# Kernel tuning notes

Measured on AMD Instinct MI355X. Metric: run time of the kernel, lower is better.

The kernel has to match this reference:

```python
import jax, jax.numpy as jnp
import numpy as np

B, P, E, D, A, M, V, T = 64, 196, 2048, 512, 512, 512, 10000, 31


def setup_inputs() -> dict:
    key = jax.random.key(0)
    ks = jax.random.split(key, 20)
    s = 0.02
    inp = {
        "encoder_out": jax.random.normal(ks[0], (B, P, E), jnp.float32),
        "captions": jax.random.randint(ks[1], (B, T), 0, V),
        "caption_lengths": jax.random.randint(ks[2], (B,), 2, T + 1).at[0].set(T),
        # parameters
        "W_emb": jax.random.normal(ks[3], (V, M), jnp.float32) * s,
        "We": jax.random.normal(ks[4], (A, E), jnp.float32) * s,
        "be": jnp.zeros((A,), jnp.float32),
        "Wd": jax.random.normal(ks[5], (A, D), jnp.float32) * s,
        "bd": jnp.zeros((A,), jnp.float32),
        "wf": jax.random.normal(ks[6], (1, A), jnp.float32) * s,
        "bf": jnp.zeros((1,), jnp.float32),
        "Wih": jax.random.normal(ks[7], (4 * D, M + E), jnp.float32) * s,
        "bih": jnp.zeros((4 * D,), jnp.float32),
        "Whh": jax.random.normal(ks[8], (4 * D, D), jnp.float32) * s,
        "bhh": jnp.zeros((4 * D,), jnp.float32),
        "Wfc": jax.random.normal(ks[9], (V, D), jnp.float32) * s,
        "bfc": jnp.zeros((V,), jnp.float32),
        "Wh0": jax.random.normal(ks[10], (D, E), jnp.float32) * s,
        "bh0": jnp.zeros((D,), jnp.float32),
        "Wc0": jax.random.normal(ks[11], (D, E), jnp.float32) * s,
        "bc0": jnp.zeros((D,), jnp.float32),
    }
    return inp


def _decode(encoder_out, W_emb, We, be, Wd, bd, wf, bf, Wih, bih, Whh, bhh,
            Wfc, bfc, Wh0, bh0, Wc0, bc0, captions, caption_lengths):
    # sort by length descending (matches torch .sort(descending=True))
    idx = jnp.argsort(-caption_lengths)
    lens = caption_lengths[idx]
    enc = encoder_out[idx]              # [B,P,E]
    caps = captions[idx]                # [B,T]
    emb = W_emb[caps]                   # [B,T,M]
    mean_enc = enc.mean(axis=1)         # [B,E]
    h0 = mean_enc @ Wh0.T + bh0         # [B,D]
    c0 = mean_enc @ Wc0.T + bc0
    dec_len = lens - 1                  # [B]
    att1 = enc @ We.T + be              # [B,P,A] precomputed encoder projection
    Tmax = caps.shape[1] - 1

    def step(carry, xs):
        h, c = carry
        e_t, t = xs                     # e_t: [B,M]
        active = (t < dec_len)          # [B]
        att2 = h @ Wd.T + bd            # [B,A]
        scores = jnp.tanh(att1 + att2[:, None, :]) @ wf[0] + bf[0]  # [B,P]
        alpha = jax.nn.softmax(scores, axis=-1)                      # [B,P]
        ctx = jnp.einsum('bp,bpe->be', alpha, enc)                   # [B,E]
        x = jnp.concatenate([e_t, ctx], axis=-1)                     # [B,M+E]
        gates = x @ Wih.T + bih + h @ Whh.T + bhh                    # [B,4D]
        i_g, f_g, g_g, o_g = jnp.split(gates, 4, axis=-1)
        c_t = jax.nn.sigmoid(f_g) * c + jax.nn.sigmoid(i_g) * jnp.tanh(g_g)
        h_t = jax.nn.sigmoid(o_g) * jnp.tanh(c_t)
        pred = h_t @ Wfc.T + bfc        # dropout in eval mode = identity
        m = active[:, None]
        h_new = jnp.where(m, h_t, h)
        c_new = jnp.where(m, c_t, c)
        pred = jnp.where(m, pred, 0.0)
        alpha = jnp.where(m, alpha, 0.0)
        return (h_new, c_new), (pred, alpha)

    emb_ts = jnp.swapaxes(emb[:, :Tmax, :], 0, 1)  # [Tmax,B,M]
    ts = jnp.arange(Tmax)
    _, (preds, alphas) = jax.lax.scan(step, (h0, c0), (emb_ts, ts))
    predictions = jnp.swapaxes(preds, 0, 1)   # [B,Tmax,V]
    alphas = jnp.swapaxes(alphas, 0, 1)       # [B,Tmax,P]
    return predictions, alphas


def reference(encoder_out, captions, caption_lengths, W_emb, We, be, Wd, bd,
              wf, bf, Wih, bih, Whh, bhh, Wfc, bfc, Wh0, bh0, Wc0, bc0):
    return _decode(encoder_out, W_emb, We, be, Wd, bd, wf, bf, Wih, bih,
                   Whh, bhh, Wfc, bfc, Wh0, bh0, Wc0, bc0,
                   captions, caption_lengths)
```

## Files before the change

### kernel.cpp

```cpp
#include <hip/hip_runtime.h>
#include <cstdint>
#include <cstddef>

typedef __attribute__((ext_vector_type(8))) short short8;
typedef __attribute__((ext_vector_type(4))) float f32x4;

#define DEV static __device__ __forceinline__

#define PRED_ELEMS 19200000ULL

#define OFF_ENC   0ULL
#define OFF_ATT1  51380224ULL
#define OFF_B1    64225280ULL
#define OFF_WFC   69468160ULL
#define OFF_WEB   79724544ULL
#define OFF_B0    81821696ULL
#define OFF_HH    81821696ULL
#define OFF_B2    86016000ULL
#define OFF_HX    94404608ULL
#define OFF_C     94535680ULL
#define OFF_ATT2  94666752ULL
#define OFF_GEH   94797824ULL
#define OFF_SC    95322112ULL
#define OFF_CTX   95372288ULL
#define OFF_META  95634432ULL
#define OFF_ENCW  96000000ULL
#define ENCW_BYTES 51380224ULL

DEV float b2f(unsigned short u){ unsigned v = ((unsigned)u) << 16; float f; __builtin_memcpy(&f, &v, 4); return f; }
DEV unsigned short f2b(float x){ unsigned v; __builtin_memcpy(&v, &x, 4); unsigned r = v + 0x7fffu + ((v >> 16) & 1u); return (unsigned short)(r >> 16); }
DEV float sigm(float x){ return 1.0f / (1.0f + __expf(-x)); }
DEV float tanhf_fast(float x){ float e = __expf(2.0f * x); return 1.0f - 2.0f / (e + 1.0f); }

DEV void gload16(const void* g, void* l){
  __builtin_amdgcn_global_load_lds((const __attribute__((address_space(1))) unsigned int*)g,
                                   (__attribute__((address_space(3))) unsigned int*)l, 16, 0, 0);
}

DEV void mm_core(const unsigned short* A, int ldA, int m0,
                 const unsigned short* Bm, int ldB, int n0,
                 int kIters, unsigned short* As, unsigned short* Bs, f32x4 acc[4])
{
  const int tid = threadIdx.x;
  const int lane = tid & 63, w = tid >> 6;
  const unsigned short* ga = A + (size_t)(m0 + lane) * ldA + w * 8;
  const unsigned short* gb = Bm + (size_t)(n0 + lane) * ldB + w * 8;
  unsigned short* la = As + w * 512;
  unsigned short* lb = Bs + w * 512;
  const int kb = lane >> 4, rr = lane & 15;
  for (int kk = 0; kk < kIters; ++kk) {
    gload16(ga, la); gload16(gb, lb);
    ga += 32; gb += 32;
    asm volatile("s_waitcnt vmcnt(0)" ::: "memory");
    __syncthreads();
    short8 bfr = *(const short8*)(Bs + (size_t)(kb * 64 + w * 16 + rr) * 8);
#pragma unroll
    for (int f = 0; f < 4; ++f) {
      short8 afr = *(const short8*)(As + (size_t)(kb * 64 + f * 16 + rr) * 8);
      acc[f] = __builtin_amdgcn_mfma_f32_16x16x32_bf16(afr, bfr, acc[f], 0, 0, 0);
    }
    __syncthreads();
  }
}

__global__ void k_meta(const int* __restrict__ caps, const int* __restrict__ lens, int* __restrict__ meta){
  int j = threadIdx.x;
  int lj = lens[j];
  int rank = 0;
  for (int k = 0; k < 64; ++k) { int lk = lens[k]; rank += (lk > lj) || (lk == lj && k < j); }
  meta[rank] = j; meta[64 + rank] = lj - 1;
  for (int t = 0; t < 31; ++t) meta[160 + rank * 31 + t] = caps[j * 31 + t];
  __syncthreads();
  if (j < 30) { int c = 0; for (int b = 0; b < 64; ++b) c += (meta[64 + b] > j); meta[128 + j] = c; }
}

__global__ __launch_bounds__(256) void k_encg(const float* __restrict__ enc, const int* __restrict__ meta, unsigned short* __restrict__ encb){
  int row = blockIdx.x; int b = row / 196, p = row % 196;
  const float* src = enc + ((size_t)meta[b] * 196 + p) * 2048;
  unsigned short* dst = encb + (size_t)row * 2048;
  int e0 = threadIdx.x * 8;
  short8 o;
#pragma unroll
  for (int j = 0; j < 8; ++j) o[j] = (short)f2b(src[e0 + j]);
  *(short8*)(dst + e0) = o;
}

__global__ __launch_bounds__(256) void k_wconv(const float* We, const float* Wh0, const float* Wc0,
                        const float* Wd, const float* Whh, const float* Wih, const float* Wfc,
                        unsigned short* Web, unsigned short* B0, unsigned short* B1,
                        unsigned short* Wfcb, unsigned short* B2){
  int bid = blockIdx.x, tid = threadIdx.x;
  if (bid < 512) {
    const float* s = We + (size_t)bid * 2048; unsigned short* d = Web + (size_t)bid * 2048;
    int e0 = tid * 8; short8 o;
#pragma unroll
    for (int j = 0; j < 8; ++j) o[j] = (short)f2b(s[e0 + j]);
    *(short8*)(d + e0) = o;
  } else if (bid < 1536) {
    int r = bid - 512;
    const float* s = (r < 512) ? (Wh0 + (size_t)r * 2048) : (Wc0 + (size_t)(r - 512) * 2048);
    unsigned short* d = B0 + (size_t)r * 2048;
    int e0 = tid * 8; short8 o;
#pragma unroll
    for (int j = 0; j < 8; ++j) o[j] = (short)f2b(s[e0 + j]);
    *(short8*)(d + e0) = o;
  } else if (bid < 3584) {
    int jr = bid - 1536; int g = (jr & 3) * 512 + (jr >> 2);
    const float* s = Wih + (size_t)g * 2560 + 512;
    unsigned short* d = B2 + (size_t)jr * 2048;
    int e0 = tid * 8; short8 o;
#pragma unroll
    for (int j = 0; j < 8; ++j) o[j] = (short)f2b(s[e0 + j]);
    *(short8*)(d + e0) = o;
  } else if (bid < 6144) {
    int n = bid - 3584; unsigned short* d = B1 + (size_t)n * 1024;
    int k0 = tid * 4;
    if (n < 512) {
#pragma unroll
      for (int j = 0; j < 4; ++j) { int k = k0 + j; d[k] = (k < 512) ? f2b(Wd[(size_t)n * 512 + k]) : (unsigned short)0; }
    } else {
      int j2 = n - 512; int g = (j2 & 3) * 512 + (j2 >> 2);
#pragma unroll
      for (int j = 0; j < 4; ++j) { int k = k0 + j;
        d[k] = (k < 512) ? f2b(Whh[(size_t)g * 512 + k]) : f2b(Wih[(size_t)g * 2560 + (k - 512)]); }
    }
  } else {
    int v = bid - 6144; unsigned short* d = Wfcb + (size_t)v * 512;
    int k0 = tid * 2;
#pragma unroll
    for (int j = 0; j < 2; ++j) d[k0 + j] = (v < 10000) ? f2b(Wfc[(size_t)v * 512 + k0 + j]) : (unsigned short)0;
  }
}

__global__ __launch_bounds__(256) void k_mean(const unsigned short* __restrict__ encb, unsigned short* __restrict__ meanb){
  int b = blockIdx.y, ch = blockIdx.x;
  int e = ch * 512 + threadIdx.x * 2;
  const unsigned short* ep = encb + (size_t)b * 196 * 2048 + e;
  float s0 = 0.f, s1 = 0.f;
  for (int p = 0; p < 196; ++p) {
    unsigned u = *(const unsigned*)(ep + (size_t)p * 2048);
    s0 += b2f((unsigned short)(u & 0xffff));
    s1 += b2f((unsigned short)(u >> 16));
  }
  const float inv = 1.0f / 196.0f;
  unsigned o = ((unsigned)f2b(s1 * inv) << 16) | f2b(s0 * inv);
  *(unsigned*)(meanb + (size_t)b * 2048 + e) = o;
}

__global__ __launch_bounds__(256) void k_h0c0(const unsigned short* meanb, const unsigned short* B0,
                      const float* bh0, const float* bc0, unsigned short* hx, float* cbuf){
  __shared__ __align__(16) unsigned short As[2048], Bs[2048];
  f32x4 acc[4];
#pragma unroll
  for (int f = 0; f < 4; ++f) acc[f] = (f32x4){0.f,0.f,0.f,0.f};
  int nt = blockIdx.x;
  mm_core(meanb, 2048, 0, B0, 2048, nt * 64, 64, As, Bs, acc);
  int lane = threadIdx.x & 63, w = threadIdx.x >> 6;
  int col = lane & 15, rhi = lane >> 4;
  int n = nt * 64 + w * 16 + col;
#pragma unroll
  for (int f = 0; f < 4; ++f)
#pragma unroll
    for (int r = 0; r < 4; ++r) {
      int b = f * 16 + rhi * 4 + r; float v = acc[f][r];
      if (n < 512) hx[(size_t)b * 1024 + n] = f2b(v + bh0[n]);
      else cbuf[(size_t)b * 512 + (n - 512)] = v + bc0[n - 512];
    }
}

__global__ void k_emb0(const float* __restrict__ Wemb, const int* __restrict__ meta, unsigned short* __restrict__ hx){
  int b = blockIdx.x;
  int cap = meta[160 + b * 31];
  for (int j = threadIdx.x; j < 512; j += 256)
    hx[(size_t)b * 1024 + 512 + j] = f2b(Wemb[(size_t)cap * 512 + j]);
}

__global__ __launch_bounds__(256) void k_att1(const unsigned short* __restrict__ encb,
                      const unsigned short* __restrict__ Web,
                      const float* __restrict__ be, unsigned short* __restrict__ att1b){
  __shared__ __align__(16) unsigned short As[2][4096], Bs[2][4096];
  int tid = threadIdx.x, lane = tid & 63, w = tid >> 6;
  int bid = blockIdx.x, mt, nt;
  if (bid < 384) { mt = (bid >> 5) * 8 + (bid & 7); nt = (bid >> 3) & 3; }
  else           { mt = 96 + ((bid - 384) >> 2);    nt = (bid - 384) & 3; }
  int wr = (w >> 1) * 64, wc = (w & 1) * 64;
  int rr = lane & 15, kb = lane >> 4;
  f32x4 acc[4][4];
#pragma unroll
  for (int f = 0; f < 4; ++f)
#pragma unroll
    for (int q = 0; q < 4; ++q) acc[f][q] = (f32x4){0.f,0.f,0.f,0.f};

  const unsigned short* gA = encb + (size_t)mt * 128 * 2048;
  const unsigned short* gB = Web + (size_t)nt * 128 * 2048;
  int L0 = tid, L1 = tid + 256;
  size_t s0 = (size_t)(L0 & 127) * 2048 + ((L0 >> 7) << 3);
  size_t s1 = (size_t)(L1 & 127) * 2048 + ((L1 >> 7) << 3);
  int d0 = (w * 64) * 8, d1 = (w * 64 + 256) * 8;

#define STAGE_A1(kk, bf) do { \
    gload16(gA + s0 + (size_t)(kk) * 32, &As[bf][d0]); \
    gload16(gB + s0 + (size_t)(kk) * 32, &Bs[bf][d0]); \
    gload16(gA + s1 + (size_t)(kk) * 32, &As[bf][d1]); \
    gload16(gB + s1 + (size_t)(kk) * 32, &Bs[bf][d1]); \
  } while (0)

  STAGE_A1(0, 0);
  __syncthreads();
  for (int kk = 0; kk < 64; ++kk) {
    int cur = kk & 1;
    if (kk < 63) STAGE_A1(kk + 1, cur ^ 1);
    short8 af[4], bq[4];
#pragma unroll
    for (int f = 0; f < 4; ++f)
      af[f] = *(const short8*)&As[cur][((kb << 7) + wr + f * 16 + rr) * 8];
#pragma unroll
    for (int q = 0; q < 4; ++q)
      bq[q] = *(const short8*)&Bs[cur][((kb << 7) + wc + q * 16 + rr) * 8];
#pragma unroll
    for (int f = 0; f < 4; ++f)
#pragma unroll
      for (int q = 0; q < 4; ++q)
        acc[f][q] = __builtin_amdgcn_mfma_f32_16x16x32_bf16(af[f], bq[q], acc[f][q], 0, 0, 0);
    __syncthreads();
  }
#undef STAGE_A1
  int col = lane & 15, rhi = lane >> 4;
#pragma unroll
  for (int q = 0; q < 4; ++q) {
    int n = nt * 128 + wc + q * 16 + col;
    float bev = be[n];
#pragma unroll
    for (int f = 0; f < 4; ++f)
#pragma unroll
      for (int r = 0; r < 4; ++r) {
        int m = mt * 128 + wr + f * 16 + rhi * 4 + r;
        att1b[(size_t)m * 512 + n] = f2b(acc[f][q][r] + bev);
      }
  }
}

__global__ __launch_bounds__(256) void k_encw(const unsigned short* __restrict__ encb,
                      const unsigned short* __restrict__ B2, unsigned short* __restrict__ encW){
  __shared__ __align__(16) unsigned short As[2][4096], Bs[2][4096];
  int tid = threadIdx.x, lane = tid & 63, w = tid >> 6;
  int mt = blockIdx.x >> 4, nt = blockIdx.x & 15;
  int wr = (w >> 1) * 64, wc = (w & 1) * 64;
  int rr = lane & 15, kb = lane >> 4;
  f32x4 acc[4][4];
#pragma unroll
  for (int f = 0; f < 4; ++f)
#pragma unroll
    for (int q = 0; q < 4; ++q) acc[f][q] = (f32x4){0.f,0.f,0.f,0.f};

  const unsigned short* gA = encb + (size_t)mt * 128 * 2048;
  const unsigned short* gB = B2 + (size_t)nt * 128 * 2048;
  int L0 = tid, L1 = tid + 256;
  size_t s0 = (size_t)(L0 & 127) * 2048 + ((L0 >> 7) << 3);
  size_t s1 = (size_t)(L1 & 127) * 2048 + ((L1 >> 7) << 3);
  int d0 = (w * 64) * 8, d1 = (w * 64 + 256) * 8;

#define STAGE_W(kk, bf) do { \
    gload16(gA + s0 + (size_t)(kk) * 32, &As[bf][d0]); \
    gload16(gB + s0 + (size_t)(kk) * 32, &Bs[bf][d0]); \
    gload16(gA + s1 + (size_t)(kk) * 32, &As[bf][d1]); \
    gload16(gB + s1 + (size_t)(kk) * 32, &Bs[bf][d1]); \
  } while (0)

  STAGE_W(0, 0);
  __syncthreads();
  for (int kk = 0; kk < 64; ++kk) {
    int cur = kk & 1;
    if (kk < 63) STAGE_W(kk + 1, cur ^ 1);
    short8 af[4], bq[4];
#pragma unroll
    for (int f = 0; f < 4; ++f)
      af[f] = *(const short8*)&As[cur][((kb << 7) + wr + f * 16 + rr) * 8];
#pragma unroll
    for (int q = 0; q < 4; ++q)
      bq[q] = *(const short8*)&Bs[cur][((kb << 7) + wc + q * 16 + rr) * 8];
#pragma unroll
    for (int f = 0; f < 4; ++f)
#pragma unroll
      for (int q = 0; q < 4; ++q)
        acc[f][q] = __builtin_amdgcn_mfma_f32_16x16x32_bf16(af[f], bq[q], acc[f][q], 0, 0, 0);
    __syncthreads();
  }
#undef STAGE_W
  int col = lane & 15, rhi = lane >> 4;
#pragma unroll
  for (int q = 0; q < 4; ++q) {
    int n = nt * 128 + wc + q * 16 + col;
#pragma unroll
    for (int f = 0; f < 4; ++f)
#pragma unroll
      for (int r = 0; r < 4; ++r) {
        int m = mt * 128 + wr + f * 16 + rhi * 4 + r;
        encW[(size_t)m * 2048 + n] = f2b(acc[f][q][r]);
      }
  }
}

__global__ __launch_bounds__(256) void k_step1lite(const unsigned short* __restrict__ hx,
                       const unsigned short* __restrict__ B1,
                       const float* __restrict__ bd, const float* __restrict__ bih, const float* __restrict__ bhh,
                       float* __restrict__ att2f, float* __restrict__ geh){
  int w = threadIdx.x >> 6, lane = threadIdx.x & 63;
  int omega = blockIdx.x * 4 + w;
  int rr = lane & 15, kb8 = (lane >> 4) * 8;
  const unsigned short* pb; int kIt;
  if (omega < 32) { pb = B1 + (size_t)(omega * 16 + rr) * 1024 + kb8; kIt = 16; }
  else            { pb = B1 + (size_t)(512 + (omega - 32) * 16 + rr) * 1024 + kb8; kIt = 32; }
  const unsigned short* pa0 = hx + (size_t)rr * 1024 + kb8;
  f32x4 acc[4];
#pragma unroll
  for (int f = 0; f < 4; ++f) acc[f] = (f32x4){0.f,0.f,0.f,0.f};
#pragma unroll 4
  for (int kk = 0; kk < kIt; ++kk) {
    short8 bfr = *(const short8*)(pb + kk * 32);
#pragma unroll
    for (int f = 0; f < 4; ++f) {
      short8 afr = *(const short8*)(pa0 + (size_t)f * 16384 + kk * 32);
      acc[f] = __builtin_amdgcn_mfma_f32_16x16x32_bf16(afr, bfr, acc[f], 0, 0, 0);
    }
  }
  int col = lane & 15, rhi = lane >> 4;
  if (omega < 32) {
    int n = omega * 16 + col; float bv = bd[n];
#pragma unroll
    for (int f = 0; f < 4; ++f)
#pragma unroll
      for (int r = 0; r < 4; ++r) { int b = f * 16 + rhi * 4 + r; att2f[(size_t)b * 512 + n] = acc[f][r] + bv; }
  } else {
    int j = (omega - 32) * 16 + col; int g = (j & 3) * 512 + (j >> 2);
    float bv = bih[g] + bhh[g];
#pragma unroll
    for (int f = 0; f < 4; ++f)
#pragma unroll
      for (int r = 0; r < 4; ++r) { int b = f * 16 + rhi * 4 + r; geh[(size_t)b * 2048 + j] = acc[f][r] + bv; }
  }
}

__global__ __launch_bounds__(256) void k_scores(int t, const unsigned short* __restrict__ att1b, const float* __restrict__ att2f,
                        const float* __restrict__ wf, const float* __restrict__ bfp,
                        const int* __restrict__ meta, float* __restrict__ sc){
  int b = blockIdx.y, pc = blockIdx.x;
  if (b >= meta[128 + t]) return;
  int tid = threadIdx.x, lane = tid & 63, w = tid >> 6;
  float wfr[8], a2[8];
#pragma unroll
  for (int j = 0; j < 8; ++j) { wfr[j] = wf[lane * 8 + j]; a2[j] = att2f[(size_t)b * 512 + lane * 8 + j]; }
  float bf0 = bfp[0];
  for (int pi = w; pi < 49; pi += 4) {
    int p = pc * 49 + pi;
    short8 av = *(const short8*)(att1b + ((size_t)(b * 196 + p)) * 512 + lane * 8);
    float s = 0.f;
#pragma unroll
    for (int j = 0; j < 8; ++j) s += tanhf_fast(b2f((unsigned short)av[j]) + a2[j]) * wfr[j];
#pragma unroll
    for (int off = 32; off; off >>= 1) s += __shfl_xor(s, off);
    if (lane == 0) sc[(size_t)b * 196 + p] = s + bf0;
  }
}

__global__ __launch_bounds__(256) void k_gc(int t, const float* __restrict__ sc,
                      const unsigned short* __restrict__ encW, const float* __restrict__ geh,
                      const float* __restrict__ Wemb, const int* __restrict__ meta,
                      float* __restrict__ out, float* __restrict__ cbuf,
                      unsigned short* __restrict__ hx, unsigned short* __restrict__ hh){
  int b = blockIdx.y, ch = blockIdx.x;
  int tid = threadIdx.x, lane = tid & 63, w = tid >> 6;
  int na = meta[128 + t];
  __shared__ float sal[200];
  __shared__ float red[256];
  __shared__ float part[4][512];
  __shared__ float gt[512];

  if (b < na) {
    float v = (tid < 196) ? sc[(size_t)b * 196 + tid] : -3.0e38f;
    red[tid] = v; __syncthreads();
    for (int s = 128; s; s >>= 1) { if (tid < s) red[tid] = fmaxf(red[tid], red[tid + s]); __syncthreads(); }
    float mx = red[0]; __syncthreads();
    float ex = (tid < 196) ? __expf(v - mx) : 0.f;
    red[tid] = ex; __syncthreads();
    for (int s = 128; s; s >>= 1) { if (tid < s) red[tid] += red[tid + s]; __syncthreads(); }
    float inv = 1.0f / red[0];
    __syncthreads();
    if (tid < 196) {
      float al = ex * inv;
      sal[tid] = al;
      if (ch == 0) out[PRED_ELEMS + ((size_t)b * 30 + t) * 196 + tid] = al;
    }
    __syncthreads();

    const unsigned short* ep = encW + ((size_t)b * 196) * 2048 + ch * 512 + lane * 8;
    float s8[8];
#pragma unroll
    for (int j = 0; j < 8; ++j) s8[j] = 0.f;
#pragma unroll 7
    for (int i = 0; i < 49; ++i) {
      int p = w + i * 4;
      short8 vv = *(const short8*)(ep + (size_t)p * 2048);
      float a = sal[p];
#pragma unroll
      for (int j = 0; j < 8; ++j) s8[j] += a * b2f((unsigned short)vv[j]);
    }
#pragma unroll
    for (int j = 0; j < 8; ++j) part[w][lane * 8 + j] = s8[j];
    __syncthreads();
    int j0 = tid * 2;
    gt[j0]     = part[0][j0] + part[1][j0] + part[2][j0] + part[3][j0]
               + geh[(size_t)b * 2048 + ch * 512 + j0];
    gt[j0 + 1] = part[0][j0 + 1] + part[1][j0 + 1] + part[2][j0 + 1] + part[3][j0 + 1]
               + geh[(size_t)b * 2048 + ch * 512 + j0 + 1];
    __syncthreads();

    if (tid < 128) {
      int d = ch * 128 + tid;
      float ig = gt[tid * 4 + 0];
      float fg = gt[tid * 4 + 1];
      float gg = gt[tid * 4 + 2];
      float og = gt[tid * 4 + 3];
      float c0 = cbuf[(size_t)b * 512 + d];
      float ct = sigm(fg) * c0 + sigm(ig) * tanhf_fast(gg);
      float ht = sigm(og) * tanhf_fast(ct);
      cbuf[(size_t)b * 512 + d] = ct;
      unsigned short hb = f2b(ht);
      hx[(size_t)b * 1024 + d] = hb;
      hh[((size_t)t * 64 + b) * 512 + d] = hb;
      int cap = meta[160 + b * 31 + t + 1];
      hx[(size_t)b * 1024 + 512 + d] = f2b(Wemb[(size_t)cap * 512 + d]);
    }
  } else {
    if (tid < 128) {
      int d = ch * 128 + tid;
      unsigned short hold = hx[(size_t)b * 1024 + d];
      hh[((size_t)t * 64 + b) * 512 + d] = hold;
      int cap = meta[160 + b * 31 + t + 1];
      hx[(size_t)b * 1024 + 512 + d] = f2b(Wemb[(size_t)cap * 512 + d]);
    }
  }
}

__global__ __launch_bounds__(256) void k_ctx(int t, const float* __restrict__ sc, const unsigned short* __restrict__ encb,
                     const int* __restrict__ meta, float* __restrict__ out, unsigned short* __restrict__ ctxb){
  int b = blockIdx.y, ch = blockIdx.x;
  if (b >= meta[128 + t]) return;
  int tid = threadIdx.x;
  __shared__ float red[256];
  __shared__ float sal[200];
  __shared__ float part[4][512];
  float v = (tid < 196) ? sc[(size_t)b * 196 + tid] : -3.0e38f;
  red[tid] = v; __syncthreads();
  for (int s = 128; s; s >>= 1) { if (tid < s) red[tid] = fmaxf(red[tid], red[tid + s]); __syncthreads(); }
  float mx = red[0]; __syncthreads();
  float ex = (tid < 196) ? __expf(v - mx) : 0.f;
  red[tid] = ex; __syncthreads();
  for (int s = 128; s; s >>= 1) { if (tid < s) red[tid] += red[tid + s]; __syncthreads(); }
  float inv = 1.0f / red[0];
  if (tid < 196) {
    float al = ex * inv;
    sal[tid] = al;
    if (ch == 0) out[PRED_ELEMS + ((size_t)b * 30 + t) * 196 + tid] = al;
  }
  __syncthreads();
  int w = tid >> 6, lane = tid & 63;
  const unsigned short* ep = encb + (size_t)b * 196 * 2048 + ch * 512 + lane * 8;
  float s8[8];
#pragma unroll
  for (int j = 0; j < 8; ++j) s8[j] = 0.f;
#pragma unroll 7
  for (int i = 0; i < 49; ++i) {
    int p = w + i * 4;
    short8 vv = *(const short8*)(ep + (size_t)p * 2048);
    float a = sal[p];
#pragma unroll
    for (int j = 0; j < 8; ++j) s8[j] += a * b2f((unsigned short)vv[j]);
  }
#pragma unroll
  for (int j = 0; j < 8; ++j) part[w][lane * 8 + j] = s8[j];
  __syncthreads();
  float r0 = part[0][tid * 2] + part[1][tid * 2] + part[2][tid * 2] + part[3][tid * 2];
  float r1 = part[0][tid * 2 + 1] + part[1][tid * 2 + 1] + part[2][tid * 2 + 1] + part[3][tid * 2 + 1];
  unsigned o = ((unsigned)f2b(r1) << 16) | f2b(r0);
  *(unsigned*)(ctxb + (size_t)b * 2048 + ch * 512 + tid * 2) = o;
}

__global__ __launch_bounds__(256) void k_step2(int t, const unsigned short* __restrict__ ctxb,
                       const unsigned short* __restrict__ B2, const float* __restrict__ geh,
                       const float* __restrict__ Wemb, const int* __restrict__ meta,
                       float* __restrict__ cbuf, unsigned short* __restrict__ hx,
                       unsigned short* __restrict__ hh){
  __shared__ float red[4][64][17];
  int w = threadIdx.x >> 6, lane = threadIdx.x & 63;
  int n0 = blockIdx.x * 16;
  int rr = lane & 15, kb8 = (lane >> 4) * 8;
  const unsigned short* pb = B2 + (size_t)(n0 + rr) * 2048 + w * 512 + kb8;
  const unsigned short* pa = ctxb + (size_t)rr * 2048 + w * 512 + kb8;
  f32x4 acc[4];
#pragma unroll
  for (int f = 0; f < 4; ++f) acc[f] = (f32x4){0.f,0.f,0.f,0.f};
#pragma unroll 4
  for (int kk = 0; kk < 16; ++kk) {
    short8 bfr = *(const short8*)(pb + kk * 32);
#pragma unroll
    for (int f = 0; f < 4; ++f) {
      short8 afr = *(const short8*)(pa + (size_t)f * 32768 + kk * 32);
      acc[f] = __builtin_amdgcn_mfma_f32_16x16x32_bf16(afr, bfr, acc[f], 0, 0, 0);
    }
  }
  int col = lane & 15, rhi = lane >> 4;
#pragma unroll
  for (int f = 0; f < 4; ++f)
#pragma unroll
    for (int r = 0; r < 4; ++r) red[w][f * 16 + rhi * 4 + r][col] = acc[f][r];
  __syncthreads();
  int b = threadIdx.x >> 2, dl = threadIdx.x & 3;
  int d = blockIdx.x * 4 + dl;
  float g4[4];
#pragma unroll
  for (int q = 0; q < 4; ++q) {
    int nl = dl * 4 + q;
    g4[q] = red[0][b][nl] + red[1][b][nl] + red[2][b][nl] + red[3][b][nl]
          + geh[(size_t)b * 2048 + n0 + nl];
  }
  float c0 = cbuf[(size_t)b * 512 + d];
  float ct = sigm(g4[1]) * c0 + sigm(g4[0]) * tanhf_fast(g4[2]);
  float ht = sigm(g4[3]) * tanhf_fast(ct);
  int na = meta[128 + t];
  unsigned short hold = hx[(size_t)b * 1024 + d];
  unsigned short hnew = (b < na) ? f2b(ht) : hold;
  if (b < na) { cbuf[(size_t)b * 512 + d] = ct; hx[(size_t)b * 1024 + d] = hnew; }
  hh[((size_t)t * 64 + b) * 512 + d] = hnew;
  int cap = meta[160 + b * 31 + t + 1];
  hx[(size_t)b * 1024 + 512 + d] = f2b(Wemb[(size_t)cap * 512 + d]);
}

__global__ __launch_bounds__(256) void k_pred(const unsigned short* __restrict__ hh,
                      const unsigned short* __restrict__ Wfcb, const float* __restrict__ bfc,
                      const int* __restrict__ meta, float* __restrict__ out){
  __shared__ __align__(16) unsigned short As[2][4096], Bs[2][4096];
  int tid = threadIdx.x, lane = tid & 63, w = tid >> 6;
  int mt = blockIdx.x % 15, nt = blockIdx.x / 15;
  int wr = (w >> 1) * 64, wc = (w & 1) * 64;
  int rr = lane & 15, kb = lane >> 4;
  f32x4 acc[4][4];
#pragma unroll
  for (int f = 0; f < 4; ++f)
#pragma unroll
    for (int q = 0; q < 4; ++q) acc[f][q] = (f32x4){0.f,0.f,0.f,0.f};

  const unsigned short* gA = hh + (size_t)mt * 128 * 512;
  int L0 = tid, L1 = tid + 256;
  size_t sa0 = (size_t)(L0 & 127) * 512 + ((L0 >> 7) << 3);
  size_t sa1 = (size_t)(L1 & 127) * 512 + ((L1 >> 7) << 3);
  int br0 = nt * 128 + (L0 & 127); if (br0 > 10015) br0 = 10015;
  int br1 = nt * 128 + (L1 & 127); if (br1 > 10015) br1 = 10015;
  size_t sb0 = (size_t)br0 * 512 + ((L0 >> 7) << 3);
  size_t sb1 = (size_t)br1 * 512 + ((L1 >> 7) << 3);
  int d0 = (w * 64) * 8, d1 = (w * 64 + 256) * 8;

#define STAGE_P(kk, bf) do { \
    gload16(gA + sa0 + (size_t)(kk) * 32, &As[bf][d0]); \
    gload16(Wfcb + sb0 + (size_t)(kk) * 32, &Bs[bf][d0]); \
    gload16(gA + sa1 + (size_t)(kk) * 32, &As[bf][d1]); \
    gload16(Wfcb + sb1 + (size_t)(kk) * 32, &Bs[bf][d1]); \
  } while (0)

  STAGE_P(0, 0);
  __syncthreads();
  for (int kk = 0; kk < 16; ++kk) {
    int cur = kk & 1;
    if (kk < 15) STAGE_P(kk + 1, cur ^ 1);
    short8 af[4], bq[4];
#pragma unroll
    for (int f = 0; f < 4; ++f)
      af[f] = *(const short8*)&As[cur][((kb << 7) + wr + f * 16 + rr) * 8];
#pragma unroll
    for (int q = 0; q < 4; ++q)
      bq[q] = *(const short8*)&Bs[cur][((kb << 7) + wc + q * 16 + rr) * 8];
#pragma unroll
    for (int f = 0; f < 4; ++f)
#pragma unroll
      for (int q = 0; q < 4; ++q)
        acc[f][q] = __builtin_amdgcn_mfma_f32_16x16x32_bf16(af[f], bq[q], acc[f][q], 0, 0, 0);
    __syncthreads();
  }
#undef STAGE_P
  int col = lane & 15, rhi = lane >> 4;
  int tt = mt * 2 + (wr >> 6);
  int na = meta[128 + tt];
#pragma unroll
  for (int q = 0; q < 4; ++q) {
    int n = nt * 128 + wc + q * 16 + col;
    if (n >= 10000) continue;
    float bv = bfc[n];
#pragma unroll
    for (int f = 0; f < 4; ++f)
#pragma unroll
      for (int r = 0; r < 4; ++r) {
        int b = f * 16 + rhi * 4 + r;
        if (b < na) out[(size_t)b * 300000 + (size_t)tt * 10000 + n] = acc[f][q][r] + bv;
      }
  }
}

extern "C" void kernel_launch(void* const* d_in, const int* in_sizes, int n_in,
                              void* d_out, int out_size, void* d_ws, size_t ws_size,
                              hipStream_t stream) {
  (void)in_sizes; (void)n_in;
  const float* enc  = (const float*)d_in[0];
  const int*   caps = (const int*)d_in[1];
  const int*   lens = (const int*)d_in[2];
  const float* Wemb = (const float*)d_in[3];
  const float* We   = (const float*)d_in[4];
  const float* be   = (const float*)d_in[5];
  const float* Wd   = (const float*)d_in[6];
  const float* bd   = (const float*)d_in[7];
  const float* wf   = (const float*)d_in[8];
  const float* bf   = (const float*)d_in[9];
  const float* Wih  = (const float*)d_in[10];
  const float* bih  = (const float*)d_in[11];
  const float* Whh  = (const float*)d_in[12];
  const float* bhh  = (const float*)d_in[13];
  const float* Wfc  = (const float*)d_in[14];
  const float* bfc  = (const float*)d_in[15];
  const float* Wh0  = (const float*)d_in[16];
  const float* bh0  = (const float*)d_in[17];
  const float* Wc0  = (const float*)d_in[18];
  const float* bc0  = (const float*)d_in[19];

  char* ws = (char*)d_ws;
  unsigned short* encb  = (unsigned short*)(ws + OFF_ENC);
  unsigned short* att1b = (unsigned short*)(ws + OFF_ATT1);
  unsigned short* B1    = (unsigned short*)(ws + OFF_B1);
  unsigned short* Wfcb  = (unsigned short*)(ws + OFF_WFC);
  unsigned short* Web   = (unsigned short*)(ws + OFF_WEB);
  unsigned short* B0    = (unsigned short*)(ws + OFF_B0);
  unsigned short* hh    = (unsigned short*)(ws + OFF_HH);
  unsigned short* B2    = (unsigned short*)(ws + OFF_B2);
  unsigned short* hx    = (unsigned short*)(ws + OFF_HX);
  float*          cbuf  = (float*)(ws + OFF_C);
  float*          att2f = (float*)(ws + OFF_ATT2);
  float*          geh   = (float*)(ws + OFF_GEH);
  float*          sc    = (float*)(ws + OFF_SC);
  unsigned short* ctxb  = (unsigned short*)(ws + OFF_CTX);
  int*            meta  = (int*)(ws + OFF_META);
  unsigned short* encWb = (unsigned short*)(ws + OFF_ENCW);
  unsigned short* meanb = ctxb;
  float* out = (float*)d_out;

  const bool useEncW = (ws_size >= OFF_ENCW + ENCW_BYTES);

  hipMemsetAsync(d_out, 0, (size_t)out_size * sizeof(float), stream);
  k_meta<<<1, 64, 0, stream>>>(caps, lens, meta);
  k_encg<<<12544, 256, 0, stream>>>(enc, meta, encb);
  k_wconv<<<16160, 256, 0, stream>>>(We, Wh0, Wc0, Wd, Whh, Wih, Wfc, Web, B0, B1, Wfcb, B2);
  k_mean<<<dim3(4, 64), 256, 0, stream>>>(encb, meanb);
  k_h0c0<<<16, 256, 0, stream>>>(meanb, B0, bh0, bc0, hx, cbuf);
  k_emb0<<<64, 256, 0, stream>>>(Wemb, meta, hx);
  k_att1<<<392, 256, 0, stream>>>(encb, Web, be, att1b);
  if (useEncW) k_encw<<<1568, 256, 0, stream>>>(encb, B2, encWb);

  for (int t = 0; t < 30; ++t) {
    k_step1lite<<<40, 256, 0, stream>>>(hx, B1, bd, bih, bhh, att2f, geh);
    k_scores<<<dim3(4, 64), 256, 0, stream>>>(t, att1b, att2f, wf, bf, meta, sc);
    if (useEncW) {
      k_gc<<<dim3(4, 64), 256, 0, stream>>>(t, sc, encWb, geh, Wemb, meta, out, cbuf, hx, hh);
    } else {
      k_ctx<<<dim3(4, 64), 256, 0, stream>>>(t, sc, encb, meta, out, ctxb);
      k_step2<<<128, 256, 0, stream>>>(t, ctxb, B2, geh, Wemb, meta, cbuf, hx, hh);
    }
  }
  k_pred<<<1185, 256, 0, stream>>>(hh, Wfcb, bfc, meta, out);
}
```

Baseline: 1.804 ms.

## Fuse attention projection, scores and softmax per batch row; swizzle encW tiles by XCD

Each decode step now runs the decoder-attention projection (att2), the attention scores and the softmax inside one kernel, one block per batch row. The gate precompute runs in extra blocks of the same launch. This removes one launch per step and the global round trip of att2 and the raw scores, while k_gc only reads the finished alphas. The fallback path without encW is dropped and the encW GEMM grid is remapped so M-tiles are spread across the 8 XCDs. In exchange, each row block recomputes a small slice of the GEMM with less parallelism, and the code now assumes the workspace is large enough.

```diff
diff --git a/kernel.cpp b/kernel.cpp
--- a/kernel.cpp
+++ b/kernel.cpp
@@ -244,7 +244,10 @@
                       const unsigned short* __restrict__ B2, unsigned short* __restrict__ encW){
   __shared__ __align__(16) unsigned short As[2][4096], Bs[2][4096];
   int tid = threadIdx.x, lane = tid & 63, w = tid >> 6;
-  int mt = blockIdx.x >> 4, nt = blockIdx.x & 15;
+  int xcd = blockIdx.x & 7, slot = blockIdx.x >> 3;
+  int mtl = slot >> 4, nt = slot & 15;
+  int mt = mtl * 8 + xcd;
+  if (mt >= 98) return;
   int wr = (w >> 1) * 64, wc = (w & 1) * 64;
   int rr = lane & 15, kb = lane >> 4;
   f32x4 acc[4][4];
@@ -301,83 +304,88 @@
   }
 }
 
-__global__ __launch_bounds__(256) void k_step1lite(const unsigned short* __restrict__ hx,
-                       const unsigned short* __restrict__ B1,
-                       const float* __restrict__ bd, const float* __restrict__ bih, const float* __restrict__ bhh,
-                       float* __restrict__ att2f, float* __restrict__ geh){
-  int w = threadIdx.x >> 6, lane = threadIdx.x & 63;
-  int omega = blockIdx.x * 4 + w;
+__global__ __launch_bounds__(256) void k_as(int t, const unsigned short* __restrict__ hx,
+                      const unsigned short* __restrict__ B1, const unsigned short* __restrict__ att1b,
+                      const float* __restrict__ bd, const float* __restrict__ bih, const float* __restrict__ bhh,
+                      const float* __restrict__ wf, const float* __restrict__ bfp,
+                      const int* __restrict__ meta,
+                      float* __restrict__ geh, float* __restrict__ out, float* __restrict__ alp){
+  int bid = blockIdx.x;
+  int tid = threadIdx.x, lane = tid & 63, w = tid >> 6;
   int rr = lane & 15, kb8 = (lane >> 4) * 8;
-  const unsigned short* pb; int kIt;
-  if (omega < 32) { pb = B1 + (size_t)(omega * 16 + rr) * 1024 + kb8; kIt = 16; }
-  else            { pb = B1 + (size_t)(512 + (omega - 32) * 16 + rr) * 1024 + kb8; kIt = 32; }
-  const unsigned short* pa0 = hx + (size_t)rr * 1024 + kb8;
-  f32x4 acc[4];
-#pragma unroll
-  for (int f = 0; f < 4; ++f) acc[f] = (f32x4){0.f,0.f,0.f,0.f};
+  if (bid >= 64) {
+    int omega = 32 + (bid - 64);
+    const unsigned short* pb = B1 + (size_t)(512 + (omega - 32) * 16 + rr) * 1024 + kb8;
+    const unsigned short* pa0 = hx + (size_t)rr * 1024 + kb8;
+    f32x4 acc[4];
+#pragma unroll
+    for (int f = 0; f < 4; ++f) acc[f] = (f32x4){0.f,0.f,0.f,0.f};
 #pragma unroll 4
-  for (int kk = 0; kk < kIt; ++kk) {
-    short8 bfr = *(const short8*)(pb + kk * 32);
-#pragma unroll
-    for (int f = 0; f < 4; ++f) {
-      short8 afr = *(const short8*)(pa0 + (size_t)f * 16384 + kk * 32);
-      acc[f] = __builtin_amdgcn_mfma_f32_16x16x32_bf16(afr, bfr, acc[f], 0, 0, 0);
-    }
-  }
-  int col = lane & 15, rhi = lane >> 4;
-  if (omega < 32) {
-    int n = omega * 16 + col; float bv = bd[n];
-#pragma unroll
-    for (int f = 0; f < 4; ++f)
-#pragma unroll
-      for (int r = 0; r < 4; ++r) { int b = f * 16 + rhi * 4 + r; att2f[(size_t)b * 512 + n] = acc[f][r] + bv; }
-  } else {
+    for (int kk = 0; kk < 32; ++kk) {
+      short8 bfr = *(const short8*)(pb + kk * 32);
+#pragma unroll
+      for (int f = 0; f < 4; ++f) {
+        short8 afr = *(const short8*)(pa0 + (size_t)f * 16384 + kk * 32);
+        acc[f] = __builtin_amdgcn_mfma_f32_16x16x32_bf16(afr, bfr, acc[f], 0, 0, 0);
+      }
+    }
+    int col = lane & 15, rhi = lane >> 4;
     int j = (omega - 32) * 16 + col; int g = (j & 3) * 512 + (j >> 2);
     float bv = bih[g] + bhh[g];
 #pragma unroll
     for (int f = 0; f < 4; ++f)
 #pragma unroll
       for (int r = 0; r < 4; ++r) { int b = f * 16 + rhi * 4 + r; geh[(size_t)b * 2048 + j] = acc[f][r] + bv; }
-  }
-}
-
-__global__ __launch_bounds__(256) void k_scores(int t, const unsigned short* __restrict__ att1b, const float* __restrict__ att2f,
-                        const float* __restrict__ wf, const float* __restrict__ bfp,
-                        const int* __restrict__ meta, float* __restrict__ sc){
-  int b = blockIdx.y, pc = blockIdx.x;
+    return;
+  }
+  int b = bid;
   if (b >= meta[128 + t]) return;
-  int tid = threadIdx.x, lane = tid & 63, w = tid >> 6;
-  float wfr[8], a2[8];
-#pragma unroll
-  for (int j = 0; j < 8; ++j) { wfr[j] = wf[lane * 8 + j]; a2[j] = att2f[(size_t)b * 512 + lane * 8 + j]; }
-  float bf0 = bfp[0];
-  for (int pi = w; pi < 49; pi += 4) {
-    int p = pc * 49 + pi;
-    short8 av = *(const short8*)(att1b + ((size_t)(b * 196 + p)) * 512 + lane * 8);
-    float s = 0.f;
-#pragma unroll
-    for (int j = 0; j < 8; ++j) s += tanhf_fast(b2f((unsigned short)av[j]) + a2[j]) * wfr[j];
-#pragma unroll
-    for (int off = 32; off; off >>= 1) s += __shfl_xor(s, off);
-    if (lane == 0) sc[(size_t)b * 196 + p] = s + bf0;
-  }
-}
-
-__global__ __launch_bounds__(256) void k_gc(int t, const float* __restrict__ sc,
-                      const unsigned short* __restrict__ encW, const float* __restrict__ geh,
-                      const float* __restrict__ Wemb, const int* __restrict__ meta,
-                      float* __restrict__ out, float* __restrict__ cbuf,
-                      unsigned short* __restrict__ hx, unsigned short* __restrict__ hh){
-  int b = blockIdx.y, ch = blockIdx.x;
-  int tid = threadIdx.x, lane = tid & 63, w = tid >> 6;
-  int na = meta[128 + t];
+  __shared__ float a2s[512];
   __shared__ float sal[200];
   __shared__ float red[256];
-  __shared__ float part[4][512];
-  __shared__ float gt[512];
-
-  if (b < na) {
-    float v = (tid < 196) ? sc[(size_t)b * 196 + tid] : -3.0e38f;
+  {
+    const unsigned short* pa = hx + (size_t)b * 1024 + kb8;
+    f32x4 acc[8];
+#pragma unroll
+    for (int q = 0; q < 8; ++q) acc[q] = (f32x4){0.f,0.f,0.f,0.f};
+#pragma unroll 4
+    for (int kk = 0; kk < 16; ++kk) {
+      short8 afr = *(const short8*)(pa + kk * 32);
+#pragma unroll
+      for (int q = 0; q < 8; ++q) {
+        const unsigned short* pb = B1 + (size_t)(w * 128 + q * 16 + rr) * 1024 + kb8;
+        short8 bfr = *(const short8*)(pb + kk * 32);
+        acc[q] = __builtin_amdgcn_mfma_f32_16x16x32_bf16(afr, bfr, acc[q], 0, 0, 0);
+      }
+    }
+    if (lane < 16) {
+#pragma unroll
+      for (int q = 0; q < 8; ++q) {
+        int n = w * 128 + q * 16 + lane;
+        a2s[n] = acc[q][0] + bd[n];
+      }
+    }
+  }
+  __syncthreads();
+  {
+    float wfr[8], a2[8];
+#pragma unroll
+    for (int j = 0; j < 8; ++j) { wfr[j] = wf[lane * 8 + j]; a2[j] = a2s[lane * 8 + j]; }
+    float bf0 = bfp[0];
+    for (int i = 0; i < 49; ++i) {
+      int p = i * 4 + w;
+      short8 av = *(const short8*)(att1b + ((size_t)(b * 196 + p)) * 512 + lane * 8);
+      float s = 0.f;
+#pragma unroll
+      for (int j = 0; j < 8; ++j) s += tanhf_fast(b2f((unsigned short)av[j]) + a2[j]) * wfr[j];
+#pragma unroll
+      for (int off = 32; off; off >>= 1) s += __shfl_xor(s, off);
+      if (lane == 0) sal[p] = s + bf0;
+    }
+  }
+  __syncthreads();
+  {
+    float v = (tid < 196) ? sal[tid] : -3.0e38f;
     red[tid] = v; __syncthreads();
     for (int s = 128; s; s >>= 1) { if (tid < s) red[tid] = fmaxf(red[tid], red[tid + s]); __syncthreads(); }
     float mx = red[0]; __syncthreads();
@@ -385,14 +393,29 @@
     red[tid] = ex; __syncthreads();
     for (int s = 128; s; s >>= 1) { if (tid < s) red[tid] += red[tid + s]; __syncthreads(); }
     float inv = 1.0f / red[0];
-    __syncthreads();
     if (tid < 196) {
       float al = ex * inv;
-      sal[tid] = al;
-      if (ch == 0) out[PRED_ELEMS + ((size_t)b * 30 + t) * 196 + tid] = al;
-    }
-    __syncthreads();
-
+      alp[(size_t)b * 196 + tid] = al;
+      out[PRED_ELEMS + ((size_t)b * 30 + t) * 196 + tid] = al;
+    }
+  }
+}
+
+__global__ __launch_bounds__(256) void k_gc(int t, const float* __restrict__ alp,
+                      const unsigned short* __restrict__ encW, const float* __restrict__ geh,
+                      const float* __restrict__ Wemb, const int* __restrict__ meta,
+                      float* __restrict__ cbuf, unsigned short* __restrict__ hx,
+                      unsigned short* __restrict__ hh){
+  int b = blockIdx.y, ch = blockIdx.x;
+  int tid = threadIdx.x, lane = tid & 63, w = tid >> 6;
+  int na = meta[128 + t];
+  __shared__ float sal[200];
+  __shared__ float part[4][512];
+  __shared__ float gt[512];
+
+  if (b < na) {
+    if (tid < 196) sal[tid] = alp[(size_t)b * 196 + tid];
+    __syncthreads();
     const unsigned short* ep = encW + ((size_t)b * 196) * 2048 + ch * 512 + lane * 8;
     float s8[8];
 #pragma unroll
@@ -442,100 +465,6 @@
   }
 }
 
-__global__ __launch_bounds__(256) void k_ctx(int t, const float* __restrict__ sc, const unsigned short* __restrict__ encb,
-                     const int* __restrict__ meta, float* __restrict__ out, unsigned short* __restrict__ ctxb){
-  int b = blockIdx.y, ch = blockIdx.x;
-  if (b >= meta[128 + t]) return;
-  int tid = threadIdx.x;
-  __shared__ float red[256];
-  __shared__ float sal[200];
-  __shared__ float part[4][512];
-  float v = (tid < 196) ? sc[(size_t)b * 196 + tid] : -3.0e38f;
-  red[tid] = v; __syncthreads();
-  for (int s = 128; s; s >>= 1) { if (tid < s) red[tid] = fmaxf(red[tid], red[tid + s]); __syncthreads(); }
-  float mx = red[0]; __syncthreads();
-  float ex = (tid < 196) ? __expf(v - mx) : 0.f;
-  red[tid] = ex; __syncthreads();
-  for (int s = 128; s; s >>= 1) { if (tid < s) red[tid] += red[tid + s]; __syncthreads(); }
-  float inv = 1.0f / red[0];
-  if (tid < 196) {
-    float al = ex * inv;
-    sal[tid] = al;
-    if (ch == 0) out[PRED_ELEMS + ((size_t)b * 30 + t) * 196 + tid] = al;
-  }
-  __syncthreads();
-  int w = tid >> 6, lane = tid & 63;
-  const unsigned short* ep = encb + (size_t)b * 196 * 2048 + ch * 512 + lane * 8;
-  float s8[8];
-#pragma unroll
-  for (int j = 0; j < 8; ++j) s8[j] = 0.f;
-#pragma unroll 7
-  for (int i = 0; i < 49; ++i) {
-    int p = w + i * 4;
-    short8 vv = *(const short8*)(ep + (size_t)p * 2048);
-    float a = sal[p];
-#pragma unroll
-    for (int j = 0; j < 8; ++j) s8[j] += a * b2f((unsigned short)vv[j]);
-  }
-#pragma unroll
-  for (int j = 0; j < 8; ++j) part[w][lane * 8 + j] = s8[j];
-  __syncthreads();
-  float r0 = part[0][tid * 2] + part[1][tid * 2] + part[2][tid * 2] + part[3][tid * 2];
-  float r1 = part[0][tid * 2 + 1] + part[1][tid * 2 + 1] + part[2][tid * 2 + 1] + part[3][tid * 2 + 1];
-  unsigned o = ((unsigned)f2b(r1) << 16) | f2b(r0);
-  *(unsigned*)(ctxb + (size_t)b * 2048 + ch * 512 + tid * 2) = o;
-}
-
-__global__ __launch_bounds__(256) void k_step2(int t, const unsigned short* __restrict__ ctxb,
-                       const unsigned short* __restrict__ B2, const float* __restrict__ geh,
-                       const float* __restrict__ Wemb, const int* __restrict__ meta,
-                       float* __restrict__ cbuf, unsigned short* __restrict__ hx,
-                       unsigned short* __restrict__ hh){
-  __shared__ float red[4][64][17];
-  int w = threadIdx.x >> 6, lane = threadIdx.x & 63;
-  int n0 = blockIdx.x * 16;
-  int rr = lane & 15, kb8 = (lane >> 4) * 8;
-  const unsigned short* pb = B2 + (size_t)(n0 + rr) * 2048 + w * 512 + kb8;
-  const unsigned short* pa = ctxb + (size_t)rr * 2048 + w * 512 + kb8;
-  f32x4 acc[4];
-#pragma unroll
-  for (int f = 0; f < 4; ++f) acc[f] = (f32x4){0.f,0.f,0.f,0.f};
-#pragma unroll 4
-  for (int kk = 0; kk < 16; ++kk) {
-    short8 bfr = *(const short8*)(pb + kk * 32);
-#pragma unroll
-    for (int f = 0; f < 4; ++f) {
-      short8 afr = *(const short8*)(pa + (size_t)f * 32768 + kk * 32);
-      acc[f] = __builtin_amdgcn_mfma_f32_16x16x32_bf16(afr, bfr, acc[f], 0, 0, 0);
-    }
-  }
-  int col = lane & 15, rhi = lane >> 4;
-#pragma unroll
-  for (int f = 0; f < 4; ++f)
-#pragma unroll
-    for (int r = 0; r < 4; ++r) red[w][f * 16 + rhi * 4 + r][col] = acc[f][r];
-  __syncthreads();
-  int b = threadIdx.x >> 2, dl = threadIdx.x & 3;
-  int d = blockIdx.x * 4 + dl;
-  float g4[4];
-#pragma unroll
-  for (int q = 0; q < 4; ++q) {
-    int nl = dl * 4 + q;
-    g4[q] = red[0][b][nl] + red[1][b][nl] + red[2][b][nl] + red[3][b][nl]
-          + geh[(size_t)b * 2048 + n0 + nl];
-  }
-  float c0 = cbuf[(size_t)b * 512 + d];
-  float ct = sigm(g4[1]) * c0 + sigm(g4[0]) * tanhf_fast(g4[2]);
-  float ht = sigm(g4[3]) * tanhf_fast(ct);
-  int na = meta[128 + t];
-  unsigned short hold = hx[(size_t)b * 1024 + d];
-  unsigned short hnew = (b < na) ? f2b(ht) : hold;
-  if (b < na) { cbuf[(size_t)b * 512 + d] = ct; hx[(size_t)b * 1024 + d] = hnew; }
-  hh[((size_t)t * 64 + b) * 512 + d] = hnew;
-  int cap = meta[160 + b * 31 + t + 1];
-  hx[(size_t)b * 1024 + 512 + d] = f2b(Wemb[(size_t)cap * 512 + d]);
-}
-
 __global__ __launch_bounds__(256) void k_pred(const unsigned short* __restrict__ hh,
                       const unsigned short* __restrict__ Wfcb, const float* __restrict__ bfc,
                       const int* __restrict__ meta, float* __restrict__ out){
@@ -608,7 +537,7 @@
 extern "C" void kernel_launch(void* const* d_in, const int* in_sizes, int n_in,
                               void* d_out, int out_size, void* d_ws, size_t ws_size,
                               hipStream_t stream) {
-  (void)in_sizes; (void)n_in;
+  (void)in_sizes; (void)n_in; (void)ws_size;
   const float* enc  = (const float*)d_in[0];
   const int*   caps = (const int*)d_in[1];
   const int*   lens = (const int*)d_in[2];
@@ -641,7 +570,6 @@
   unsigned short* B2    = (unsigned short*)(ws + OFF_B2);
   unsigned short* hx    = (unsigned short*)(ws + OFF_HX);
   float*          cbuf  = (float*)(ws + OFF_C);
-  float*          att2f = (float*)(ws + OFF_ATT2);
   float*          geh   = (float*)(ws + OFF_GEH);
   float*          sc    = (float*)(ws + OFF_SC);
   unsigned short* ctxb  = (unsigned short*)(ws + OFF_CTX);
@@ -649,8 +577,6 @@
   unsigned short* encWb = (unsigned short*)(ws + OFF_ENCW);
   unsigned short* meanb = ctxb;
   float* out = (float*)d_out;
-
-  const bool useEncW = (ws_size >= OFF_ENCW + ENCW_BYTES);
 
   hipMemsetAsync(d_out, 0, (size_t)out_size * sizeof(float), stream);
   k_meta<<<1, 64, 0, stream>>>(caps, lens, meta);
@@ -660,17 +586,11 @@
   k_h0c0<<<16, 256, 0, stream>>>(meanb, B0, bh0, bc0, hx, cbuf);
   k_emb0<<<64, 256, 0, stream>>>(Wemb, meta, hx);
   k_att1<<<392, 256, 0, stream>>>(encb, Web, be, att1b);
-  if (useEncW) k_encw<<<1568, 256, 0, stream>>>(encb, B2, encWb);
+  k_encw<<<1664, 256, 0, stream>>>(encb, B2, encWb);
 
   for (int t = 0; t < 30; ++t) {
-    k_step1lite<<<40, 256, 0, stream>>>(hx, B1, bd, bih, bhh, att2f, geh);
-    k_scores<<<dim3(4, 64), 256, 0, stream>>>(t, att1b, att2f, wf, bf, meta, sc);
-    if (useEncW) {
-      k_gc<<<dim3(4, 64), 256, 0, stream>>>(t, sc, encWb, geh, Wemb, meta, out, cbuf, hx, hh);
-    } else {
-      k_ctx<<<dim3(4, 64), 256, 0, stream>>>(t, sc, encb, meta, out, ctxb);
-      k_step2<<<128, 256, 0, stream>>>(t, ctxb, B2, geh, Wemb, meta, cbuf, hx, hh);
-    }
+    k_as<<<192, 256, 0, stream>>>(t, hx, B1, att1b, bd, bih, bhh, wf, bf, meta, geh, out, sc);
+    k_gc<<<dim3(4, 64), 256, 0, stream>>>(t, sc, encWb, geh, Wemb, meta, cbuf, hx, hh);
   }
   k_pred<<<1185, 256, 0, stream>>>(hh, Wfcb, bfc, meta, out);
 }
```

Measured after the change: 2.722 ms. +50.9%, slower.
